# Optimization experiments

Hardware: AMD Instinct MI355X
Metric: run time of the kernel (lower is better)

Reference implementation:

```python
import jax, jax.numpy as jnp
import numpy as np

L, H, E, V, N, VOCAB = 6, 16, 1024, 32, 4096, 32000
D_SQRT = float(np.sqrt(V))


def _positions(n, e):
    # Faithful to source: exponent uses d = max_context_size (n), and the
    # ternary is INSIDE sin(): even i -> sin(x), odd i -> sin(cos(x)).
    pos = np.arange(n, dtype=np.float64)[:, None]
    i = np.arange(e, dtype=np.float64)[None, :]
    x = pos / (10000.0 ** (2.0 * i / n))
    arr = np.where((np.arange(e)[None, :] % 2) == 0, np.sin(x), np.sin(np.cos(x)))
    return jnp.asarray(arr, dtype=jnp.float32)


def setup_inputs() -> dict:
    key = jax.random.key(0)
    ks = jax.random.split(key, 10)
    context = jax.random.randint(ks[0], (N,), 0, VOCAB)
    table = jax.random.normal(ks[1], (VOCAB, E), dtype=jnp.float32)
    pos = _positions(N, E)
    # torch.rand-style uniform weights, scaled small for numerical sanity
    Wq = jax.random.uniform(ks[2], (L, H, E, V), dtype=jnp.float32) * 0.05
    Wk = jax.random.uniform(ks[3], (L, H, E, V), dtype=jnp.float32) * 0.05
    Wv = jax.random.uniform(ks[4], (L, H, E, V), dtype=jnp.float32) * 0.05
    Wo = jax.random.uniform(ks[5], (L, H * V, E), dtype=jnp.float32) * 0.05
    W1 = jax.random.normal(ks[6], (L, E, 2 * E), dtype=jnp.float32) * 0.02
    b1 = jnp.zeros((L, 2 * E), dtype=jnp.float32)
    W2 = jax.random.normal(ks[7], (L, 2 * E, E), dtype=jnp.float32) * 0.02
    b2 = jnp.zeros((L, E), dtype=jnp.float32)
    return {"context": context, "table": table, "pos": pos, "Wq": Wq, "Wk": Wk,
            "Wv": Wv, "Wo": Wo, "W1": W1, "b1": b1, "W2": W2, "b2": b2}


def _layernorm(x):
    # source LayerNorm: mean/std over dim=1, unbiased std (ddof=1), no eps
    m = jnp.mean(x, axis=1, keepdims=True)
    s = jnp.std(x, axis=1, ddof=1, keepdims=True)
    return (x - m) / s


def _block(z, p):
    wq, wk, wv, wo, w1, bb1, w2, bb2 = p
    q = jnp.einsum('ne,hev->hnv', z, wq)
    k = jnp.einsum('ne,hev->hnv', z, wk)
    v = jnp.einsum('ne,hev->hnv', z, wv)
    att = jax.nn.softmax(jnp.einsum('hnv,hmv->hnm', q, k) / D_SQRT, axis=-1)
    o = jnp.einsum('hnm,hmv->nhv', att, v).reshape(z.shape[0], -1)  # concat heads on dim 1
    an = _layernorm(z + o @ wo)
    ff = jax.nn.leaky_relu(an @ w1 + bb1, 0.01) @ w2 + bb2
    return _layernorm(an + ff), None


def reference(context, table, pos, Wq, Wk, Wv, Wo, W1, b1, W2, b2):
    z0 = table[context] + pos  # [N, E]
    z, _ = jax.lax.scan(_block, z0, (Wq, Wk, Wv, Wo, W1, b1, W2, b2))
    return z
```

## Files before the change

### kernel.cpp

```cpp
#include <hip/hip_runtime.h>
#include <hip/hip_bf16.h>

typedef _Float16 f16;
typedef __attribute__((ext_vector_type(8))) _Float16 f16x8;
typedef __attribute__((ext_vector_type(4))) float f4v;
typedef __attribute__((ext_vector_type(16))) float f32x16;

constexpr int NSEQ = 4096;
constexpr int EMB  = 1024;
constexpr int NH   = 16;
constexpr int HD   = 32;
constexpr int NL   = 6;
constexpr int HV   = NH * HD;
constexpr int FF   = 2 * EMB;
constexpr int QKVW = 3 * HV;

#define GLDS16(gp, lp) __builtin_amdgcn_global_load_lds( \
    (const __attribute__((address_space(1))) void*)(const void*)(gp), \
    (__attribute__((address_space(3))) void*)(void*)(lp), 16, 0, 0)

__device__ __forceinline__ unsigned pk2h(float a, float b) {
  auto h = __builtin_amdgcn_cvt_pkrtz(a, b);
  unsigned d; __builtin_memcpy(&d, &h, 4);
  return d;
}

__global__ __launch_bounds__(256) void embed_kernel(const int* __restrict__ ctx,
    const float* __restrict__ table, const float* __restrict__ pos,
    float* __restrict__ z, f16* __restrict__ zh){
  int t = blockIdx.x * 256 + threadIdx.x;
  int n = t >> 8;
  int e = (t & 255) << 2;
  float4 a = *reinterpret_cast<const float4*>(table + (size_t)ctx[n] * EMB + e);
  float4 b = *reinterpret_cast<const float4*>(pos   + (size_t)n * EMB + e);
  float4 r = {a.x + b.x, a.y + b.y, a.z + b.z, a.w + b.w};
  *reinterpret_cast<float4*>(z + (size_t)n * EMB + e) = r;
  f16 o[4] = {(f16)r.x, (f16)r.y, (f16)r.z, (f16)r.w};
  uint2 u; __builtin_memcpy(&u, o, 8);
  *reinterpret_cast<uint2*>(zh + (size_t)n * EMB + e) = u;
}

__global__ __launch_bounds__(256) void convT_kernel(const float* __restrict__ in,
    f16* __restrict__ out, int K, int N, long sInZ, long sOutZ){
  __shared__ float t[32][33];
  in  += (size_t)blockIdx.z * sInZ;
  out += (size_t)blockIdx.z * sOutZ;
  int k0 = blockIdx.x * 32, n0 = blockIdx.y * 32;
  int r = threadIdx.x >> 5, c = threadIdx.x & 31;
  #pragma unroll
  for (int i = 0; i < 4; i++)
    t[r + i*8][c] = in[(size_t)(k0 + r + i*8) * N + n0 + c];
  __syncthreads();
  #pragma unroll
  for (int i = 0; i < 4; i++)
    out[(size_t)(n0 + r + i*8) * K + k0 + c] = (f16)t[c][r + i*8];
}

template<typename CT>
__global__ __launch_bounds__(256) void gemm_mfma(
    const f16* __restrict__ A, const f16* __restrict__ Bt, CT* C,
    const float* __restrict__ bias, const float* res,
    int K, int Nc, int leaky)
{
  __shared__ f16 Ash[128 * 32];
  __shared__ f16 Bsh[128 * 32];
  int tid = threadIdx.x;
  int lane = tid & 63, w = tid >> 6;
  int wm = w & 1, wn = w >> 1;
  int l16 = lane & 15, quad = lane >> 4;
  int row0 = blockIdx.y * 128, col0 = blockIdx.x * 128;

  f4v acc[4][4];
  #pragma unroll
  for (int i = 0; i < 4; i++)
    #pragma unroll
    for (int j = 0; j < 4; j++) acc[i][j] = {0.f, 0.f, 0.f, 0.f};

  int srow = lane >> 2;
  int scol = (lane & 3) * 8;
  const f16* gA0 = A  + (size_t)(row0 + w*32      + srow) * K + scol;
  const f16* gA1 = A  + (size_t)(row0 + w*32 + 16 + srow) * K + scol;
  const f16* gB0 = Bt + (size_t)(col0 + w*32      + srow) * K + scol;
  const f16* gB1 = Bt + (size_t)(col0 + w*32 + 16 + srow) * K + scol;
  f16* lA0 = Ash + (w*2    ) * 512;
  f16* lA1 = Ash + (w*2 + 1) * 512;
  f16* lB0 = Bsh + (w*2    ) * 512;
  f16* lB1 = Bsh + (w*2 + 1) * 512;

  for (int k0 = 0; k0 < K; k0 += 32) {
    __syncthreads();
    GLDS16(gA0 + k0, lA0);
    GLDS16(gA1 + k0, lA1);
    GLDS16(gB0 + k0, lB0);
    GLDS16(gB1 + k0, lB1);
    __syncthreads();
    f16x8 af[4], bf[4];
    #pragma unroll
    for (int mt = 0; mt < 4; mt++)
      af[mt] = *reinterpret_cast<const f16x8*>(&Ash[(wm*64 + mt*16 + l16) * 32 + quad*8]);
    #pragma unroll
    for (int nt = 0; nt < 4; nt++)
      bf[nt] = *reinterpret_cast<const f16x8*>(&Bsh[(wn*64 + nt*16 + l16) * 32 + quad*8]);
    #pragma unroll
    for (int mt = 0; mt < 4; mt++)
      #pragma unroll
      for (int nt = 0; nt < 4; nt++)
        acc[mt][nt] = __builtin_amdgcn_mfma_f32_16x16x32_f16(af[mt], bf[nt], acc[mt][nt], 0, 0, 0);
  }

  #pragma unroll
  for (int mt = 0; mt < 4; mt++) {
    #pragma unroll
    for (int nt = 0; nt < 4; nt++) {
      int ccol = col0 + wn*64 + nt*16 + l16;
      float bv = bias ? bias[ccol] : 0.f;
      #pragma unroll
      for (int reg = 0; reg < 4; reg++) {
        int crow = row0 + wm*64 + mt*16 + quad*4 + reg;
        float v = acc[mt][nt][reg] + bv;
        if (leaky) v = v > 0.f ? v : 0.01f * v;
        if (res)   v += res[(size_t)crow * Nc + ccol];
        if constexpr (sizeof(CT) == 2) C[(size_t)crow * Nc + ccol] = (f16)v;
        else                           C[(size_t)crow * Nc + ccol] = v;
      }
    }
  }
}

__global__ __launch_bounds__(128) void attn_mfma(const f16* __restrict__ qkv,
    f16* __restrict__ O)
{
  __shared__ f16 Ks[2][128][40];
  __shared__ f16 Vt[2][32][136];
  int tid = threadIdx.x;
  int lane = tid & 63, w = tid >> 6;
  int l31 = lane & 31, h = lane >> 5;
  int hd = blockIdx.y;
  int q0 = blockIdx.x * 64 + w * 32;
  const float sc = 0.17677669529663687f * 1.4426950408889634f;

  f16x8 qf0, qf1;
  {
    const f16* qp = qkv + (size_t)(q0 + l31) * QKVW + hd * HD + h * 8;
    union { uint4 u; f16 e[8]; } a, b;
    a.u = *reinterpret_cast<const uint4*>(qp);
    b.u = *reinterpret_cast<const uint4*>(qp + 16);
    #pragma unroll
    for (int i = 0; i < 8; i++) {
      a.e[i] = (f16)((float)a.e[i] * sc);
      b.e[i] = (f16)((float)b.e[i] * sc);
    }
    __builtin_memcpy(&qf0, a.e, 16);
    __builtin_memcpy(&qf1, b.e, 16);
  }

  float m_ = -1e30f, lsum = 0.f;
  f32x16 oaccA, oaccB, zz;
  #pragma unroll
  for (int i = 0; i < 16; i++) { oaccA[i] = 0.f; oaccB[i] = 0.f; zz[i] = 0.f; }

  int vkp = tid & 63;
  uint4 kr0, kr1, kr2, kr3, vr0, vr1, vr2, vr3;

  auto LOADT = [&](int kt) {
    const f16* kp = qkv + (size_t)(kt + tid) * QKVW + HV + hd * HD;
    const uint4* kq = reinterpret_cast<const uint4*>(kp);
    kr0 = kq[0]; kr1 = kq[1]; kr2 = kq[2]; kr3 = kq[3];
    const f16* vp = qkv + (size_t)(kt + 2*vkp) * QKVW + 2*HV + hd * HD + w * 16;
    vr0 = *reinterpret_cast<const uint4*>(vp);
    vr1 = *reinterpret_cast<const uint4*>(vp + QKVW);
    vr2 = *reinterpret_cast<const uint4*>(vp + 8);
    vr3 = *reinterpret_cast<const uint4*>(vp + QKVW + 8);
  };
  auto WRITET = [&](int b) {
    *reinterpret_cast<uint4*>(&Ks[b][tid][0])  = kr0;
    *reinterpret_cast<uint4*>(&Ks[b][tid][8])  = kr1;
    *reinterpret_cast<uint4*>(&Ks[b][tid][16]) = kr2;
    *reinterpret_cast<uint4*>(&Ks[b][tid][24]) = kr3;
    union { uint4 u; f16 e[8]; } c0, c1, c2, c3;
    c0.u = vr0; c1.u = vr1; c2.u = vr2; c3.u = vr3;
    #pragma unroll
    for (int i = 0; i < 8; i++) {
      f16 p0[2] = {c0.e[i], c1.e[i]};
      unsigned d0; __builtin_memcpy(&d0, p0, 4);
      *reinterpret_cast<unsigned*>(&Vt[b][w*16 + i][2*vkp]) = d0;
      f16 p1[2] = {c2.e[i], c3.e[i]};
      unsigned d1; __builtin_memcpy(&d1, p1, 4);
      *reinterpret_cast<unsigned*>(&Vt[b][w*16 + 8 + i][2*vkp]) = d1;
    }
  };

  LOADT(0);
  WRITET(0);
  __syncthreads();
  int cur = 0;

  for (int kt = 0; kt < NSEQ; kt += 128) {
    LOADT((kt + 128) & (NSEQ - 1));

    f32x16 s0, s1, s2, s3;
    __builtin_amdgcn_s_setprio(1);
    #define SCHUNK(sv, c) { \
      f16x8 a0 = *reinterpret_cast<const f16x8*>(&Ks[cur][(c)*32 + l31][h*8]); \
      f16x8 a1 = *reinterpret_cast<const f16x8*>(&Ks[cur][(c)*32 + l31][16 + h*8]); \
      sv = __builtin_amdgcn_mfma_f32_32x32x16_f16(a0, qf0, zz, 0, 0, 0); \
      sv = __builtin_amdgcn_mfma_f32_32x32x16_f16(a1, qf1, sv, 0, 0, 0); }
    SCHUNK(s0, 0) SCHUNK(s1, 1) SCHUNK(s2, 2) SCHUNK(s3, 3)
    #undef SCHUNK
    __builtin_amdgcn_s_setprio(0);

    auto cmax = [](const f32x16& s) {
      float a = fmaxf(fmaxf(s[0], s[1]),   fmaxf(s[2], s[3]));
      float b = fmaxf(fmaxf(s[4], s[5]),   fmaxf(s[6], s[7]));
      float c = fmaxf(fmaxf(s[8], s[9]),   fmaxf(s[10], s[11]));
      float d = fmaxf(fmaxf(s[12], s[13]), fmaxf(s[14], s[15]));
      return fmaxf(fmaxf(a, b), fmaxf(c, d));
    };
    float tm = fmaxf(fmaxf(cmax(s0), cmax(s1)), fmaxf(cmax(s2), cmax(s3)));
    tm = fmaxf(tm, __shfl_xor(tm, 32));
    if (!__all(tm <= m_)) {
      float mN = fmaxf(m_, tm);
      float corr = __builtin_amdgcn_exp2f(m_ - mN);
      m_ = mN; lsum *= corr;
      #pragma unroll
      for (int i = 0; i < 16; i++) { oaccA[i] *= corr; oaccB[i] *= corr; }
    }

    float ls = 0.f;
    #define PVCHUNK(sv, c, oacc) { \
      float pv[16]; \
      _Pragma("unroll") \
      for (int r_ = 0; r_ < 16; r_++) { \
        pv[r_] = __builtin_amdgcn_exp2f(sv[r_] - m_); ls += pv[r_]; } \
      unsigned d00 = pk2h(pv[0],  pv[1]),  d01 = pk2h(pv[2],  pv[3]);  \
      unsigned d10 = pk2h(pv[4],  pv[5]),  d11 = pk2h(pv[6],  pv[7]);  \
      unsigned d20 = pk2h(pv[8],  pv[9]),  d21 = pk2h(pv[10], pv[11]); \
      unsigned d30 = pk2h(pv[12], pv[13]), d31 = pk2h(pv[14], pv[15]); \
      unsigned rxA0 = (unsigned)__shfl_xor((int)(h ? d00 : d10), 32); \
      unsigned rxA1 = (unsigned)__shfl_xor((int)(h ? d01 : d11), 32); \
      unsigned rxB0 = (unsigned)__shfl_xor((int)(h ? d20 : d30), 32); \
      unsigned rxB1 = (unsigned)__shfl_xor((int)(h ? d21 : d31), 32); \
      unsigned o00 = h ? d10 : d00, o01 = h ? d11 : d01; \
      unsigned o10 = h ? d30 : d20, o11 = h ? d31 : d21; \
      unsigned fr0[4] = { h ? rxA0 : o00, h ? rxA1 : o01, \
                          h ? o00 : rxA0, h ? o01 : rxA1 }; \
      unsigned fr1[4] = { h ? rxB0 : o10, h ? rxB1 : o11, \
                          h ? o10 : rxB0, h ? o11 : rxB1 }; \
      f16x8 pb0, pb1; \
      __builtin_memcpy(&pb0, fr0, 16); __builtin_memcpy(&pb1, fr1, 16); \
      f16x8 vf0 = *reinterpret_cast<const f16x8*>(&Vt[cur][l31][(c)*32 + h*8]); \
      f16x8 vf1 = *reinterpret_cast<const f16x8*>(&Vt[cur][l31][(c)*32 + 16 + h*8]); \
      __builtin_amdgcn_s_setprio(1); \
      oacc = __builtin_amdgcn_mfma_f32_32x32x16_f16(vf0, pb0, oacc, 0, 0, 0); \
      oacc = __builtin_amdgcn_mfma_f32_32x32x16_f16(vf1, pb1, oacc, 0, 0, 0); \
      __builtin_amdgcn_s_setprio(0); }
    PVCHUNK(s0, 0, oaccA)
    PVCHUNK(s1, 1, oaccB)
    PVCHUNK(s2, 2, oaccA)
    PVCHUNK(s3, 3, oaccB)
    #undef PVCHUNK
    lsum += ls;

    if (kt + 128 < NSEQ) WRITET(cur ^ 1);
    __syncthreads();
    cur ^= 1;
  }

  lsum += __shfl_xor(lsum, 32);
  float inv = 1.f / lsum;
  f16* op = O + (size_t)(q0 + l31) * HV + hd * HD;
  #pragma unroll
  for (int g = 0; g < 4; g++) {
    f16 ob[4];
    #pragma unroll
    for (int r = 0; r < 4; r++)
      ob[r] = (f16)((oaccA[4*g + r] + oaccB[4*g + r]) * inv);
    uint2 u; __builtin_memcpy(&u, ob, 8);
    *reinterpret_cast<uint2*>(op + 8*g + 4*h) = u;
  }
}

__global__ __launch_bounds__(256) void ln_kernel(const float* in, float* out,
                                                 f16* __restrict__ outh){
  __shared__ float sm[8];
  int row = blockIdx.x, tid = threadIdx.x;
  float4 x = reinterpret_cast<const float4*>(in + (size_t)row * EMB)[tid];
  float s = x.x + x.y + x.z + x.w;
  #pragma unroll
  for (int o = 32; o > 0; o >>= 1) s += __shfl_down(s, o);
  int wid = tid >> 6, lane = tid & 63;
  if (lane == 0) sm[wid] = s;
  __syncthreads();
  float mean = (sm[0] + sm[1] + sm[2] + sm[3]) * (1.f / EMB);
  float dx = x.x - mean, dy = x.y - mean, dz = x.z - mean, dw = x.w - mean;
  float qs = dx*dx + dy*dy + dz*dz + dw*dw;
  #pragma unroll
  for (int o = 32; o > 0; o >>= 1) qs += __shfl_down(qs, o);
  if (lane == 0) sm[4 + wid] = qs;
  __syncthreads();
  float var = (sm[4] + sm[5] + sm[6] + sm[7]) * (1.f / (EMB - 1));
  float inv = rsqrtf(var);
  float4 y = {dx * inv, dy * inv, dz * inv, dw * inv};
  reinterpret_cast<float4*>(out + (size_t)row * EMB)[tid] = y;
  f16 o4[4] = {(f16)y.x, (f16)y.y, (f16)y.z, (f16)y.w};
  uint2 u; __builtin_memcpy(&u, o4, 8);
  reinterpret_cast<uint2*>(outh + (size_t)row * EMB)[tid] = u;
}

extern "C" void kernel_launch(void* const* d_in, const int* in_sizes, int n_in,
                              void* d_out, int out_size, void* d_ws, size_t ws_size,
                              hipStream_t stream)
{
  const int*   ctx   = (const int*)d_in[0];
  const float* table = (const float*)d_in[1];
  const float* pos   = (const float*)d_in[2];
  const float* Wq    = (const float*)d_in[3];
  const float* Wk    = (const float*)d_in[4];
  const float* Wv    = (const float*)d_in[5];
  const float* Wo    = (const float*)d_in[6];
  const float* W1    = (const float*)d_in[7];
  const float* b1    = (const float*)d_in[8];
  const float* W2    = (const float*)d_in[9];
  const float* b2    = (const float*)d_in[10];

  float* z = (float*)d_out;

  char* ws = (char*)d_ws;
  const size_t MB = 1u << 20;
  float* an   = (float*)(ws);
  f16*   anh  = (f16*)  (ws + 16 * MB);
  f16*   zh   = (f16*)  (ws + 24 * MB);
  f16*   qkvh = (f16*)  (ws + 32 * MB);
  f16*   Oh   = (f16*)  (ws + 44 * MB);
  f16*   h1h  = (f16*)  (ws + 32 * MB);
  f16*   wbuf = (f16*)  (ws + 48 * MB);

  embed_kernel<<<NSEQ * EMB / 4 / 256, 256, 0, stream>>>(ctx, table, pos, z, zh);

  for (int l = 0; l < NL; l++) {
    const float* wq  = Wq + (size_t)l * NH * EMB * HD;
    const float* wk  = Wk + (size_t)l * NH * EMB * HD;
    const float* wv  = Wv + (size_t)l * NH * EMB * HD;
    const float* wo  = Wo + (size_t)l * HV * EMB;
    const float* w1  = W1 + (size_t)l * EMB * FF;
    const float* bb1 = b1 + (size_t)l * FF;
    const float* w2  = W2 + (size_t)l * FF * EMB;
    const float* bb2 = b2 + (size_t)l * EMB;

    convT_kernel<<<dim3(EMB/32, 1, NH), 256, 0, stream>>>(
        wq, wbuf + (size_t)0 * HV * EMB, EMB, HD, (long)EMB * HD, (long)HD * EMB);
    convT_kernel<<<dim3(EMB/32, 1, NH), 256, 0, stream>>>(
        wk, wbuf + (size_t)1 * HV * EMB, EMB, HD, (long)EMB * HD, (long)HD * EMB);
    convT_kernel<<<dim3(EMB/32, 1, NH), 256, 0, stream>>>(
        wv, wbuf + (size_t)2 * HV * EMB, EMB, HD, (long)EMB * HD, (long)HD * EMB);
    gemm_mfma<f16><<<dim3(QKVW/128, NSEQ/128), 256, 0, stream>>>(
        zh, wbuf, qkvh, nullptr, nullptr, EMB, QKVW, 0);

    attn_mfma<<<dim3(NSEQ/64, NH), 128, 0, stream>>>(qkvh, Oh);

    convT_kernel<<<dim3(HV/32, EMB/32, 1), 256, 0, stream>>>(
        wo, wbuf, HV, EMB, 0, 0);
    gemm_mfma<float><<<dim3(EMB/128, NSEQ/128), 256, 0, stream>>>(
        Oh, wbuf, z, nullptr, z, HV, EMB, 0);
    ln_kernel<<<NSEQ, 256, 0, stream>>>(z, an, anh);

    convT_kernel<<<dim3(EMB/32, FF/32, 1), 256, 0, stream>>>(
        w1, wbuf, EMB, FF, 0, 0);
    gemm_mfma<f16><<<dim3(FF/128, NSEQ/128), 256, 0, stream>>>(
        anh, wbuf, h1h, bb1, nullptr, EMB, FF, 1);
    convT_kernel<<<dim3(FF/32, EMB/32, 1), 256, 0, stream>>>(
        w2, wbuf, FF, EMB, 0, 0);
    gemm_mfma<float><<<dim3(EMB/128, NSEQ/128), 256, 0, stream>>>(
        h1h, wbuf, z, bb2, an, FF, EMB, 0);
    ln_kernel<<<NSEQ, 256, 0, stream>>>(z, z, zh);
  }
}
```

Measured before the change: 2.017 ms.

## Split attention over two key segments with merge kernel, fuse QKV weight transposes

Attention now splits the key range into two halves along a new grid dimension. Each block uses 256 threads covering 128 queries and writes unnormalized fp32 partial outputs plus per-row max and sum. A new merge kernel combines the two halves with log-sum-exp rescaling into the f16 output, aiming for more parallelism and occupancy at the cost of extra global traffic and a launch. The three per-layer Q/K/V weight transposes are also fused into one launch.

```diff
diff --git a/kernel.cpp b/kernel.cpp
--- a/kernel.cpp
+++ b/kernel.cpp
@@ -14,6 +14,7 @@
 constexpr int HV   = NH * HD;
 constexpr int FF   = 2 * EMB;
 constexpr int QKVW = 3 * HV;
+constexpr int KSEG = NSEQ / 2;
 
 #define GLDS16(gp, lp) __builtin_amdgcn_global_load_lds( \
     (const __attribute__((address_space(1))) void*)(const void*)(gp), \
@@ -56,6 +57,24 @@
     out[(size_t)(n0 + r + i*8) * K + k0 + c] = (f16)t[c][r + i*8];
 }
 
+__global__ __launch_bounds__(256) void convT3_kernel(const float* __restrict__ wq,
+    const float* __restrict__ wk, const float* __restrict__ wv,
+    f16* __restrict__ out){
+  __shared__ float t[32][33];
+  int zz = blockIdx.z; int sec = zz >> 4, hh = zz & 15;
+  const float* in = (sec == 0 ? wq : sec == 1 ? wk : wv) + (size_t)hh * EMB * HD;
+  f16* o = out + (size_t)sec * HV * EMB + (size_t)hh * HD * EMB;
+  int k0 = blockIdx.x * 32;
+  int r = threadIdx.x >> 5, c = threadIdx.x & 31;
+  #pragma unroll
+  for (int i = 0; i < 4; i++)
+    t[r + i*8][c] = in[(size_t)(k0 + r + i*8) * HD + c];
+  __syncthreads();
+  #pragma unroll
+  for (int i = 0; i < 4; i++)
+    o[(size_t)(r + i*8) * EMB + k0 + c] = (f16)t[c][r + i*8];
+}
+
 template<typename CT>
 __global__ __launch_bounds__(256) void gemm_mfma(
     const f16* __restrict__ A, const f16* __restrict__ Bt, CT* C,
@@ -127,8 +146,8 @@
   }
 }
 
-__global__ __launch_bounds__(128) void attn_mfma(const f16* __restrict__ qkv,
-    f16* __restrict__ O)
+__global__ __launch_bounds__(256, 4) void attn_mfma(const f16* __restrict__ qkv,
+    float* __restrict__ Opart, float2* __restrict__ ml)
 {
   __shared__ f16 Ks[2][128][40];
   __shared__ f16 Vt[2][32][136];
@@ -136,7 +155,9 @@
   int lane = tid & 63, w = tid >> 6;
   int l31 = lane & 31, h = lane >> 5;
   int hd = blockIdx.y;
-  int q0 = blockIdx.x * 64 + w * 32;
+  int zseg = blockIdx.z;
+  int q0 = blockIdx.x * 128 + w * 32;
+  int base = zseg * KSEG;
   const float sc = 0.17677669529663687f * 1.4426950408889634f;
 
   f16x8 qf0, qf1;
@@ -159,44 +180,38 @@
   #pragma unroll
   for (int i = 0; i < 16; i++) { oaccA[i] = 0.f; oaccB[i] = 0.f; zz[i] = 0.f; }
 
-  int vkp = tid & 63;
-  uint4 kr0, kr1, kr2, kr3, vr0, vr1, vr2, vr3;
+  int krow = tid >> 1, kcol = (tid & 1) * 16;
+  int vkp = tid & 63, vdg = tid >> 6;
+  uint4 kr0, kr1, vr0, vr1;
 
   auto LOADT = [&](int kt) {
-    const f16* kp = qkv + (size_t)(kt + tid) * QKVW + HV + hd * HD;
-    const uint4* kq = reinterpret_cast<const uint4*>(kp);
-    kr0 = kq[0]; kr1 = kq[1]; kr2 = kq[2]; kr3 = kq[3];
-    const f16* vp = qkv + (size_t)(kt + 2*vkp) * QKVW + 2*HV + hd * HD + w * 16;
+    const f16* kp = qkv + (size_t)(kt + krow) * QKVW + HV + hd * HD + kcol;
+    kr0 = *reinterpret_cast<const uint4*>(kp);
+    kr1 = *reinterpret_cast<const uint4*>(kp + 8);
+    const f16* vp = qkv + (size_t)(kt + 2*vkp) * QKVW + 2*HV + hd * HD + vdg * 8;
     vr0 = *reinterpret_cast<const uint4*>(vp);
     vr1 = *reinterpret_cast<const uint4*>(vp + QKVW);
-    vr2 = *reinterpret_cast<const uint4*>(vp + 8);
-    vr3 = *reinterpret_cast<const uint4*>(vp + QKVW + 8);
   };
   auto WRITET = [&](int b) {
-    *reinterpret_cast<uint4*>(&Ks[b][tid][0])  = kr0;
-    *reinterpret_cast<uint4*>(&Ks[b][tid][8])  = kr1;
-    *reinterpret_cast<uint4*>(&Ks[b][tid][16]) = kr2;
-    *reinterpret_cast<uint4*>(&Ks[b][tid][24]) = kr3;
-    union { uint4 u; f16 e[8]; } c0, c1, c2, c3;
-    c0.u = vr0; c1.u = vr1; c2.u = vr2; c3.u = vr3;
+    *reinterpret_cast<uint4*>(&Ks[b][krow][kcol])     = kr0;
+    *reinterpret_cast<uint4*>(&Ks[b][krow][kcol + 8]) = kr1;
+    union { uint4 u; f16 e[8]; } c0, c1;
+    c0.u = vr0; c1.u = vr1;
     #pragma unroll
     for (int i = 0; i < 8; i++) {
-      f16 p0[2] = {c0.e[i], c1.e[i]};
-      unsigned d0; __builtin_memcpy(&d0, p0, 4);
-      *reinterpret_cast<unsigned*>(&Vt[b][w*16 + i][2*vkp]) = d0;
-      f16 p1[2] = {c2.e[i], c3.e[i]};
-      unsigned d1; __builtin_memcpy(&d1, p1, 4);
-      *reinterpret_cast<unsigned*>(&Vt[b][w*16 + 8 + i][2*vkp]) = d1;
+      f16 pr[2] = {c0.e[i], c1.e[i]};
+      unsigned d; __builtin_memcpy(&d, pr, 4);
+      *reinterpret_cast<unsigned*>(&Vt[b][vdg * 8 + i][2 * vkp]) = d;
     }
   };
 
-  LOADT(0);
+  LOADT(base);
   WRITET(0);
   __syncthreads();
   int cur = 0;
 
-  for (int kt = 0; kt < NSEQ; kt += 128) {
-    LOADT((kt + 128) & (NSEQ - 1));
+  for (int kt = base; kt < base + KSEG; kt += 128) {
+    LOADT(base + ((kt + 128 - base) & (KSEG - 1)));
 
     f32x16 s0, s1, s2, s3;
     __builtin_amdgcn_s_setprio(1);
@@ -261,23 +276,43 @@
     #undef PVCHUNK
     lsum += ls;
 
-    if (kt + 128 < NSEQ) WRITET(cur ^ 1);
+    if (kt + 128 < base + KSEG) WRITET(cur ^ 1);
     __syncthreads();
     cur ^= 1;
   }
 
-  lsum += __shfl_xor(lsum, 32);
-  float inv = 1.f / lsum;
-  f16* op = O + (size_t)(q0 + l31) * HV + hd * HD;
+  float lt = lsum + __shfl_xor(lsum, 32);
+  float* op = Opart + (((size_t)zseg * NSEQ + q0 + l31) * NH + hd) * HD;
   #pragma unroll
   for (int g = 0; g < 4; g++) {
-    f16 ob[4];
-    #pragma unroll
-    for (int r = 0; r < 4; r++)
-      ob[r] = (f16)((oaccA[4*g + r] + oaccB[4*g + r]) * inv);
-    uint2 u; __builtin_memcpy(&u, ob, 8);
-    *reinterpret_cast<uint2*>(op + 8*g + 4*h) = u;
-  }
+    float4 v4 = {oaccA[4*g+0] + oaccB[4*g+0], oaccA[4*g+1] + oaccB[4*g+1],
+                 oaccA[4*g+2] + oaccB[4*g+2], oaccA[4*g+3] + oaccB[4*g+3]};
+    *reinterpret_cast<float4*>(op + 8*g + 4*h) = v4;
+  }
+  if (h == 0)
+    ml[((size_t)zseg * NSEQ + q0 + l31) * NH + hd] = make_float2(m_, lt);
+}
+
+__global__ __launch_bounds__(256) void attn_merge(const float* __restrict__ Opart,
+    const float2* __restrict__ ml, f16* __restrict__ Oh){
+  int t = blockIdx.x * 256 + threadIdx.x;
+  int n = t >> 7;
+  int rem = t & 127;
+  int h = rem >> 3, dg = rem & 7;
+  float2 a = ml[((size_t)0 * NSEQ + n) * NH + h];
+  float2 b = ml[((size_t)1 * NSEQ + n) * NH + h];
+  float m = fmaxf(a.x, b.x);
+  float c0 = __builtin_amdgcn_exp2f(a.x - m);
+  float c1 = __builtin_amdgcn_exp2f(b.x - m);
+  float inv = 1.f / (c0 * a.y + c1 * b.y);
+  float4 o0 = *reinterpret_cast<const float4*>(
+      &Opart[(((size_t)0 * NSEQ + n) * NH + h) * HD + dg * 4]);
+  float4 o1 = *reinterpret_cast<const float4*>(
+      &Opart[(((size_t)1 * NSEQ + n) * NH + h) * HD + dg * 4]);
+  f16 ob[4] = {(f16)((c0*o0.x + c1*o1.x) * inv), (f16)((c0*o0.y + c1*o1.y) * inv),
+               (f16)((c0*o0.z + c1*o1.z) * inv), (f16)((c0*o0.w + c1*o1.w) * inv)};
+  uint2 u; __builtin_memcpy(&u, ob, 8);
+  *reinterpret_cast<uint2*>(Oh + (size_t)n * HV + h * HD + dg * 4) = u;
 }
 
 __global__ __launch_bounds__(256) void ln_kernel(const float* in, float* out,
@@ -327,13 +362,15 @@
 
   char* ws = (char*)d_ws;
   const size_t MB = 1u << 20;
-  float* an   = (float*)(ws);
-  f16*   anh  = (f16*)  (ws + 16 * MB);
-  f16*   zh   = (f16*)  (ws + 24 * MB);
-  f16*   qkvh = (f16*)  (ws + 32 * MB);
-  f16*   Oh   = (f16*)  (ws + 44 * MB);
-  f16*   h1h  = (f16*)  (ws + 32 * MB);
-  f16*   wbuf = (f16*)  (ws + 48 * MB);
+  float*  an    = (float*)(ws);
+  f16*    anh   = (f16*)  (ws + 16 * MB);
+  f16*    zh    = (f16*)  (ws + 24 * MB);
+  f16*    qkvh  = (f16*)  (ws + 32 * MB);
+  f16*    Oh    = (f16*)  (ws + 44 * MB);
+  f16*    h1h   = (f16*)  (ws + 32 * MB);
+  f16*    wbuf  = (f16*)  (ws + 48 * MB);
+  float*  Opart = (float*)(ws);
+  float2* mlb   = (float2*)(ws + 16 * MB);
 
   embed_kernel<<<NSEQ * EMB / 4 / 256, 256, 0, stream>>>(ctx, table, pos, z, zh);
 
@@ -347,16 +384,12 @@
     const float* w2  = W2 + (size_t)l * FF * EMB;
     const float* bb2 = b2 + (size_t)l * EMB;
 
-    convT_kernel<<<dim3(EMB/32, 1, NH), 256, 0, stream>>>(
-        wq, wbuf + (size_t)0 * HV * EMB, EMB, HD, (long)EMB * HD, (long)HD * EMB);
-    convT_kernel<<<dim3(EMB/32, 1, NH), 256, 0, stream>>>(
-        wk, wbuf + (size_t)1 * HV * EMB, EMB, HD, (long)EMB * HD, (long)HD * EMB);
-    convT_kernel<<<dim3(EMB/32, 1, NH), 256, 0, stream>>>(
-        wv, wbuf + (size_t)2 * HV * EMB, EMB, HD, (long)EMB * HD, (long)HD * EMB);
+    convT3_kernel<<<dim3(EMB/32, 1, 48), 256, 0, stream>>>(wq, wk, wv, wbuf);
     gemm_mfma<f16><<<dim3(QKVW/128, NSEQ/128), 256, 0, stream>>>(
         zh, wbuf, qkvh, nullptr, nullptr, EMB, QKVW, 0);
 
-    attn_mfma<<<dim3(NSEQ/64, NH), 128, 0, stream>>>(qkvh, Oh);
+    attn_mfma<<<dim3(NSEQ/128, NH, 2), 256, 0, stream>>>(qkvh, Opart, mlb);
+    attn_merge<<<NSEQ * NH * HD / 4 / 256, 256, 0, stream>>>(Opart, mlb, Oh);
 
     convT_kernel<<<dim3(HV/32, EMB/32, 1), 256, 0, stream>>>(
         wo, wbuf, HV, EMB, 0, 0);
```

After: 2.272 ms. 12.7% more time.
